# Kernel optimization log

Hardware: AMD Instinct MI355X
Metric: run time of the kernel (lower is better)

## Reference

```python
import jax, jax.numpy as jnp
import numpy as np


def setup_inputs() -> dict:
    key = jax.random.key(0)
    ks = jax.random.split(key, 7)
    B, T, K, H, A = 32, 32, 196, 512, 512
    # Xavier-normal-ish scale for square 512x512 linears
    s = float(np.sqrt(2.0 / (H + A)))
    return {
        "att_feats": jax.random.normal(ks[0], (B, K, H), jnp.float32),
        "hiddens": jax.random.normal(ks[1], (B, T, H), jnp.float32),
        "sentinel": jax.random.normal(ks[2], (B, T, H), jnp.float32),
        "Wv": jax.random.normal(ks[3], (H, A), jnp.float32) * s,
        "Wg": jax.random.normal(ks[4], (H, A), jnp.float32) * s,
        "Ws": jax.random.normal(ks[5], (H, A), jnp.float32) * s,
        "wh": jax.random.normal(ks[6], (A,), jnp.float32) * s,
    }


def reference(att_feats, hiddens, sentinel, Wv, Wg, Ws, wh):
    # Dropout treated as identity (eval mode / deterministic reference).
    cv = jnp.einsum("bkh,ha->bka", att_feats, Wv)          # [B,K,A]
    cg = jnp.einsum("bth,ha->bta", hiddens, Wg)            # [B,T,A]
    # Broadcast additive attention: [B,T,K,A]
    content_v = cv[:, None, :, :] + cg[:, :, None, :]
    z_t = jnp.einsum("btka,a->btk", jnp.tanh(content_v), wh)  # [B,T,K]
    alpha_t = jax.nn.softmax(z_t, axis=-1)                    # [B,T,K]
    c_t = jnp.einsum("btk,bkh->bth", alpha_t, att_feats)      # [B,T,H]
    # Sentinel branch
    content_s = jnp.einsum("bth,ha->bta", sentinel, Ws) + cg  # [B,T,A]
    z_ext = jnp.einsum("bta,a->bt", jnp.tanh(content_s), wh)[..., None]  # [B,T,1]
    extended = jnp.concatenate([z_t, z_ext], axis=2)          # [B,T,K+1]
    alpha_hat = jax.nn.softmax(extended, axis=-1)
    beta_t = alpha_hat[:, :, -1:]                             # [B,T,1]
    c_hat_t = beta_t * sentinel + (1.0 - beta_t) * c_t        # [B,T,H]
    return (c_hat_t, alpha_t, beta_t)
```

## Files before the change

### kernel.cpp

```cpp
#include <hip/hip_runtime.h>
#include <hip/hip_bf16.h>
#include <math.h>

#define HDIM 512
#define ADIM 512
#define BATCH 32
#define TDIM 32
#define KDIM 196
#define MROWS 8320

typedef short short8 __attribute__((ext_vector_type(8)));
typedef float floatx4 __attribute__((ext_vector_type(4)));

__device__ __forceinline__ void gl_lds16(const __hip_bfloat16* g, __hip_bfloat16* l) {
    __builtin_amdgcn_global_load_lds(
        (const __attribute__((address_space(1))) unsigned int*)(const void*)g,
        (__attribute__((address_space(3))) unsigned int*)(void*)l, 16, 0, 0);
}

__global__ __launch_bounds__(256) void convA(const float* __restrict__ att,
                                             const float* __restrict__ hid,
                                             const float* __restrict__ sen,
                                             __hip_bfloat16* __restrict__ ahi,
                                             __hip_bfloat16* __restrict__ alo) {
    const int idx = blockIdx.x * 256 + threadIdx.x;
    const int row = idx >> 7;
    float4 v;
    if (row < 6272)      v = ((const float4*)att)[idx];
    else if (row < 7296) v = ((const float4*)hid)[idx - 6272 * 128];
    else                 v = ((const float4*)sen)[idx - 7296 * 128];
    float x[4] = {v.x, v.y, v.z, v.w};
    union { __hip_bfloat16 b[4]; uint2 u; } H, L;
    #pragma unroll
    for (int i = 0; i < 4; ++i) {
        H.b[i] = __float2bfloat16(x[i]);
        L.b[i] = __float2bfloat16(x[i] - __bfloat162float(H.b[i]));
    }
    ((uint2*)ahi)[idx] = H.u;
    ((uint2*)alo)[idx] = L.u;
}

__global__ __launch_bounds__(256) void convB(const float* __restrict__ Wv,
                                             const float* __restrict__ Wg,
                                             const float* __restrict__ Ws,
                                             __hip_bfloat16* __restrict__ bthi,
                                             __hip_bfloat16* __restrict__ btlo) {
    __shared__ float tile[64][65];
    const int tid = threadIdx.x;
    const float* src = blockIdx.z == 0 ? Wv : (blockIdx.z == 1 ? Wg : Ws);
    const int k0 = blockIdx.x * 64, n0 = blockIdx.y * 64;
    #pragma unroll
    for (int i = 0; i < 16; ++i) {
        int k = (tid >> 6) * 16 + i;
        int n = tid & 63;
        tile[k][n] = src[(size_t)(k0 + k) * 512 + n0 + n];
    }
    __syncthreads();
    const size_t obase = (size_t)blockIdx.z * 262144;
    #pragma unroll
    for (int i = 0; i < 16; ++i) {
        int n = (tid >> 6) * 16 + i;
        int k = tid & 63;
        float x = tile[k][n];
        __hip_bfloat16 h = __float2bfloat16(x);
        __hip_bfloat16 l = __float2bfloat16(x - __bfloat162float(h));
        size_t o = obase + (size_t)(n0 + n) * 512 + k0 + k;
        bthi[o] = h;
        btlo[o] = l;
    }
}

__global__ __launch_bounds__(256) void gemm_bf16x3(
        const __hip_bfloat16* __restrict__ Ahi, const __hip_bfloat16* __restrict__ Alo,
        const __hip_bfloat16* __restrict__ Bthi, const __hip_bfloat16* __restrict__ Btlo,
        float* __restrict__ C) {
    __shared__ __hip_bfloat16 smem[12288];

    const int tid  = threadIdx.x;
    const int lane = tid & 63;
    const int wave = tid >> 6;
    const int wm = wave >> 1;
    const int wn = wave & 1;
    const int row0 = blockIdx.x * 64;
    const int col0 = blockIdx.y * 128;
    const int seg = (row0 < 6272) ? 0 : ((row0 < 7296) ? 1 : 2);
    const __hip_bfloat16* Bh = Bthi + (size_t)seg * 262144;
    const __hip_bfloat16* Bl = Btlo + (size_t)seg * 262144;

    floatx4 acc[2][4];
    #pragma unroll
    for (int i = 0; i < 2; ++i)
        #pragma unroll
        for (int j = 0; j < 4; ++j)
            acc[i][j] = (floatx4){0.f, 0.f, 0.f, 0.f};

    const int kq8 = (lane >> 4) << 3;

    for (int k0 = 0; k0 < 512; k0 += 32) {
        #pragma unroll
        for (int s = 0; s < 6; ++s) {
            int u = tid + (s << 8);
            __hip_bfloat16* ldst = smem + u * 8;
            const __hip_bfloat16* gsrc;
            if (u < 256)        gsrc = Ahi + (size_t)(row0 + (u >> 2)) * 512 + k0 + ((u & 3) << 3);
            else if (u < 512)   { int v = u - 256;  gsrc = Alo + (size_t)(row0 + (v >> 2)) * 512 + k0 + ((v & 3) << 3); }
            else if (u < 1024)  { int v = u - 512;  gsrc = Bh  + (size_t)(col0 + (v >> 2)) * 512 + k0 + ((v & 3) << 3); }
            else                { int v = u - 1024; gsrc = Bl  + (size_t)(col0 + (v >> 2)) * 512 + k0 + ((v & 3) << 3); }
            gl_lds16(gsrc, ldst);
        }
        asm volatile("s_waitcnt vmcnt(0)" ::: "memory");
        __syncthreads();

        short8 a_hi[2], a_lo[2], b_hi[4], b_lo[4];
        #pragma unroll
        for (int i = 0; i < 2; ++i) {
            int m = wm * 32 + i * 16 + (lane & 15);
            a_hi[i] = *(const short8*)(smem + m * 32 + kq8);
            a_lo[i] = *(const short8*)(smem + 2048 + m * 32 + kq8);
        }
        #pragma unroll
        for (int j = 0; j < 4; ++j) {
            int n = wn * 64 + j * 16 + (lane & 15);
            b_hi[j] = *(const short8*)(smem + 4096 + n * 32 + kq8);
            b_lo[j] = *(const short8*)(smem + 8192 + n * 32 + kq8);
        }

        #pragma unroll
        for (int i = 0; i < 2; ++i)
            #pragma unroll
            for (int j = 0; j < 4; ++j) {
                acc[i][j] = __builtin_amdgcn_mfma_f32_16x16x32_bf16(a_hi[i], b_hi[j], acc[i][j], 0, 0, 0);
                acc[i][j] = __builtin_amdgcn_mfma_f32_16x16x32_bf16(a_hi[i], b_lo[j], acc[i][j], 0, 0, 0);
                acc[i][j] = __builtin_amdgcn_mfma_f32_16x16x32_bf16(a_lo[i], b_hi[j], acc[i][j], 0, 0, 0);
            }
        __syncthreads();
    }

    #pragma unroll
    for (int i = 0; i < 2; ++i) {
        #pragma unroll
        for (int r = 0; r < 4; ++r) {
            int row = row0 + wm * 32 + i * 16 + ((lane >> 4) << 2) + r;
            float* cp = C + (size_t)row * 512 + col0 + wn * 64 + (lane & 15);
            #pragma unroll
            for (int j = 0; j < 4; ++j) cp[j * 16] = acc[i][j][r];
        }
    }
}

__global__ __launch_bounds__(256) void z_kernel(const float* __restrict__ cv,
                                                const float* __restrict__ cg,
                                                const float* __restrict__ cs,
                                                const float* __restrict__ wh,
                                                float* __restrict__ z_t,
                                                float* __restrict__ z_ext) {
    __shared__ float cvs[8][132];
    __shared__ float cgs[32][132];
    __shared__ float css[32][132];
    __shared__ float whs[132];
    __shared__ float2 tbl[512];

    const int kb   = blockIdx.x;
    const int b    = blockIdx.y;
    const int tid  = threadIdx.x;
    const int wave = tid >> 6;
    const int lane = tid & 63;
    const int t       = tid & 31;
    const int k_local = tid >> 5;
    const int k       = kb * 8 + k_local;
    const bool do_z = (k < KDIM);
    const bool do_s = (kb == 24) && (wave == 2) && (lane < 32);
    const bool last = (kb == 24);

    #pragma unroll
    for (int j = tid; j < 512; j += 256) {
        float x  = -8.0f + (float)j * (1.0f / 32.0f);
        float t0 = tanhf(x);
        float t1 = tanhf(x + (1.0f / 32.0f));
        tbl[j] = make_float2(t0, t1 - t0);
    }

    const int r_st = tid >> 5;
    const int q_st = tid & 31;

    float acc = 0.f, acc2 = 0.f, acc_s = 0.f, acc_s2 = 0.f;

    for (int c = 0; c < 4; ++c) {
        const int a0 = c * 128;
        __syncthreads();
        {
            int kr = kb * 8 + r_st;
            if (kr < KDIM)
                *(float4*)&cvs[r_st][4 * q_st] =
                    *(const float4*)(cv + ((size_t)b * KDIM + kr) * ADIM + a0 + 4 * q_st);
        }
        #pragma unroll
        for (int s = 0; s < 4; ++s) {
            int idx = tid + s * 256;
            int rr = idx >> 5, qq = idx & 31;
            *(float4*)&cgs[rr][4 * qq] =
                *(const float4*)(cg + ((size_t)b * TDIM + rr) * ADIM + a0 + 4 * qq);
        }
        if (last) {
            #pragma unroll
            for (int s = 0; s < 4; ++s) {
                int idx = tid + s * 256;
                int rr = idx >> 5, qq = idx & 31;
                *(float4*)&css[rr][4 * qq] =
                    *(const float4*)(cs + ((size_t)b * TDIM + rr) * ADIM + a0 + 4 * qq);
            }
        }
        if (tid < 32)
            *(float4*)&whs[4 * tid] = *(const float4*)(wh + a0 + 4 * tid);
        __syncthreads();

        if (do_z) {
            #pragma unroll 8
            for (int q = 0; q < 32; ++q) {
                float4 v  = *(const float4*)&cvs[k_local][4 * q];
                float4 g  = *(const float4*)&cgs[t][4 * q];
                float4 w4 = *(const float4*)&whs[4 * q];
                float u0 = v.x + g.x, u1 = v.y + g.y, u2 = v.z + g.z, u3 = v.w + g.w;
                float y0 = fminf(fmaxf(fmaf(u0, 32.f, 256.f), 0.f), 511.f);
                float y1 = fminf(fmaxf(fmaf(u1, 32.f, 256.f), 0.f), 511.f);
                float y2 = fminf(fmaxf(fmaf(u2, 32.f, 256.f), 0.f), 511.f);
                float y3 = fminf(fmaxf(fmaf(u3, 32.f, 256.f), 0.f), 511.f);
                int i0 = (int)y0, i1 = (int)y1, i2 = (int)y2, i3 = (int)y3;
                float f0 = y0 - (float)i0, f1 = y1 - (float)i1;
                float f2 = y2 - (float)i2, f3 = y3 - (float)i3;
                float2 s0 = tbl[i0], s1 = tbl[i1], s2 = tbl[i2], s3 = tbl[i3];
                acc  = fmaf(w4.x, fmaf(f0, s0.y, s0.x), acc);
                acc2 = fmaf(w4.y, fmaf(f1, s1.y, s1.x), acc2);
                acc  = fmaf(w4.z, fmaf(f2, s2.y, s2.x), acc);
                acc2 = fmaf(w4.w, fmaf(f3, s3.y, s3.x), acc2);
            }
        }
        if (do_s) {
            #pragma unroll 8
            for (int q = 0; q < 32; ++q) {
                float4 v  = *(const float4*)&css[lane][4 * q];
                float4 g  = *(const float4*)&cgs[lane][4 * q];
                float4 w4 = *(const float4*)&whs[4 * q];
                float u0 = v.x + g.x, u1 = v.y + g.y, u2 = v.z + g.z, u3 = v.w + g.w;
                float y0 = fminf(fmaxf(fmaf(u0, 32.f, 256.f), 0.f), 511.f);
                float y1 = fminf(fmaxf(fmaf(u1, 32.f, 256.f), 0.f), 511.f);
                float y2 = fminf(fmaxf(fmaf(u2, 32.f, 256.f), 0.f), 511.f);
                float y3 = fminf(fmaxf(fmaf(u3, 32.f, 256.f), 0.f), 511.f);
                int i0 = (int)y0, i1 = (int)y1, i2 = (int)y2, i3 = (int)y3;
                float f0 = y0 - (float)i0, f1 = y1 - (float)i1;
                float f2 = y2 - (float)i2, f3 = y3 - (float)i3;
                float2 s0 = tbl[i0], s1 = tbl[i1], s2 = tbl[i2], s3 = tbl[i3];
                acc_s  = fmaf(w4.x, fmaf(f0, s0.y, s0.x), acc_s);
                acc_s2 = fmaf(w4.y, fmaf(f1, s1.y, s1.x), acc_s2);
                acc_s  = fmaf(w4.z, fmaf(f2, s2.y, s2.x), acc_s);
                acc_s2 = fmaf(w4.w, fmaf(f3, s3.y, s3.x), acc_s2);
            }
        }
    }

    if (do_z) z_t[((size_t)b * TDIM + t) * KDIM + k] = acc + acc2;
    if (do_s) z_ext[b * TDIM + lane] = acc_s + acc_s2;
}

__global__ __launch_bounds__(256) void out_kernel(const float* __restrict__ z_t,
                                                  const float* __restrict__ z_ext,
                                                  const float* __restrict__ att,
                                                  const float* __restrict__ sen,
                                                  float* __restrict__ out_chat,
                                                  float* __restrict__ out_alpha,
                                                  float* __restrict__ out_beta) {
    __shared__ float alpha_s[4][200];
    __shared__ float beta_s[4];

    const int tg = blockIdx.x;
    const int b  = blockIdx.y;
    const int tid  = threadIdx.x;
    const int wave = tid >> 6;
    const int lane = tid & 63;
    const int t = tg * 4 + wave;

    const float* zrow = z_t + ((size_t)b * TDIM + t) * KDIM;
    float z0 = zrow[lane];
    float z1 = zrow[lane + 64];
    float z2 = zrow[lane + 128];
    float z3 = (lane < 4) ? zrow[lane + 192] : -INFINITY;

    float m = fmaxf(fmaxf(z0, z1), fmaxf(z2, z3));
    #pragma unroll
    for (int off = 32; off; off >>= 1) m = fmaxf(m, __shfl_xor(m, off, 64));

    float e0 = __expf(z0 - m), e1 = __expf(z1 - m);
    float e2 = __expf(z2 - m), e3 = (lane < 4) ? __expf(z3 - m) : 0.0f;
    float s = e0 + e1 + e2 + e3;
    #pragma unroll
    for (int off = 32; off; off >>= 1) s += __shfl_xor(s, off, 64);

    float invS = 1.0f / s;
    float a0 = e0 * invS, a1 = e1 * invS, a2 = e2 * invS, a3 = e3 * invS;

    float* arow = out_alpha + ((size_t)b * TDIM + t) * KDIM;
    alpha_s[wave][lane] = a0;        arow[lane] = a0;
    alpha_s[wave][lane + 64] = a1;   arow[lane + 64] = a1;
    alpha_s[wave][lane + 128] = a2;  arow[lane + 128] = a2;
    if (lane < 4) { alpha_s[wave][lane + 192] = a3; arow[lane + 192] = a3; }

    if (lane == 0) {
        float se = z_ext[b * TDIM + t];
        float m2 = fmaxf(m, se);
        float eext = __expf(se - m2);
        float S2 = s * __expf(m - m2) + eext;
        float beta = eext / S2;
        beta_s[wave] = beta;
        out_beta[b * TDIM + t] = beta;
    }
    __syncthreads();

    const float* attb = att + (size_t)b * KDIM * HDIM;
    float acc[4][2] = {};
    #pragma unroll 4
    for (int k = 0; k < KDIM; ++k) {
        float av0 = attb[(size_t)k * HDIM + tid];
        float av1 = attb[(size_t)k * HDIM + tid + 256];
        #pragma unroll
        for (int w = 0; w < 4; ++w) {
            float a = alpha_s[w][k];
            acc[w][0] = fmaf(a, av0, acc[w][0]);
            acc[w][1] = fmaf(a, av1, acc[w][1]);
        }
    }

    #pragma unroll
    for (int w = 0; w < 4; ++w) {
        int tt = tg * 4 + w;
        float beta = beta_s[w];
        float om = 1.0f - beta;
        size_t o = ((size_t)b * TDIM + tt) * HDIM;
        out_chat[o + tid]       = fmaf(beta, sen[o + tid],       om * acc[w][0]);
        out_chat[o + tid + 256] = fmaf(beta, sen[o + tid + 256], om * acc[w][1]);
    }
}

__global__ __launch_bounds__(256) void gemm_f32(const float* __restrict__ Amat,
                                                const float* __restrict__ Bmat,
                                                float* __restrict__ Cmat) {
    __shared__ float As[16][64 + 4];
    __shared__ float Bs[16][64];
    const int tid = threadIdx.x;
    const int tx = tid & 15;
    const int ty = tid >> 4;
    const int row0 = blockIdx.x * 64;
    const int col0 = blockIdx.y * 64;
    float acc[4][4] = {};
    for (int k0 = 0; k0 < HDIM; k0 += 16) {
        #pragma unroll
        for (int i = 0; i < 4; ++i) {
            int idx = tid + i * 256;
            As[idx & 15][idx >> 4] = Amat[(size_t)(row0 + (idx >> 4)) * HDIM + k0 + (idx & 15)];
        }
        #pragma unroll
        for (int i = 0; i < 4; ++i) {
            int idx = tid + i * 256;
            Bs[idx >> 6][idx & 63] = Bmat[(size_t)(k0 + (idx >> 6)) * ADIM + col0 + (idx & 63)];
        }
        __syncthreads();
        #pragma unroll
        for (int k = 0; k < 16; ++k) {
            float4 a4 = *(const float4*)&As[k][ty * 4];
            float4 b4 = *(const float4*)&Bs[k][tx * 4];
            float a[4] = {a4.x, a4.y, a4.z, a4.w};
            float b[4] = {b4.x, b4.y, b4.z, b4.w};
            #pragma unroll
            for (int i = 0; i < 4; ++i)
                #pragma unroll
                for (int j = 0; j < 4; ++j)
                    acc[i][j] += a[i] * b[j];
        }
        __syncthreads();
    }
    #pragma unroll
    for (int i = 0; i < 4; ++i) {
        size_t r = (size_t)(row0 + ty * 4 + i) * ADIM + col0 + tx * 4;
        #pragma unroll
        for (int j = 0; j < 4; ++j) Cmat[r + j] = acc[i][j];
    }
}

extern "C" void kernel_launch(void* const* d_in, const int* in_sizes, int n_in,
                              void* d_out, int out_size, void* d_ws, size_t ws_size,
                              hipStream_t stream) {
    const float* att = (const float*)d_in[0];
    const float* hid = (const float*)d_in[1];
    const float* sen = (const float*)d_in[2];
    const float* Wv  = (const float*)d_in[3];
    const float* Wg  = (const float*)d_in[4];
    const float* Ws  = (const float*)d_in[5];
    const float* wh  = (const float*)d_in[6];

    float* out = (float*)d_out;
    float* out_chat  = out;
    float* out_alpha = out + 524288;
    float* out_beta  = out + 524288 + 200704;

    char* wsb = (char*)d_ws;
    const size_t C_BYTES  = (size_t)MROWS * 512 * 4;
    const size_t ZT_BYTES = 200704 * 4;
    const size_t ZE_BYTES = 4096;
    const size_t AH_BYTES = (size_t)MROWS * 512 * 2;
    const size_t BT_BYTES = (size_t)3 * 512 * 512 * 2;
    const size_t need = C_BYTES + ZT_BYTES + ZE_BYTES + 2 * AH_BYTES + 2 * BT_BYTES;

    float* C  = (float*)wsb;
    float* cv = C;
    float* cg = C + 6272 * 512;
    float* cs = C + 7296 * 512;
    float* zt = (float*)(wsb + C_BYTES);
    float* ze = (float*)(wsb + C_BYTES + ZT_BYTES);

    if (ws_size >= need) {
        __hip_bfloat16* ahi  = (__hip_bfloat16*)(wsb + C_BYTES + ZT_BYTES + ZE_BYTES);
        __hip_bfloat16* alo  = ahi + (size_t)MROWS * 512;
        __hip_bfloat16* bthi = alo + (size_t)MROWS * 512;
        __hip_bfloat16* btlo = bthi + (size_t)3 * 512 * 512;

        convA<<<4160, 256, 0, stream>>>(att, hid, sen, ahi, alo);
        convB<<<dim3(8, 8, 3), 256, 0, stream>>>(Wv, Wg, Ws, bthi, btlo);
        gemm_bf16x3<<<dim3(130, 4), 256, 0, stream>>>(ahi, alo, bthi, btlo, C);
    } else {
        gemm_f32<<<dim3(98, 8), 256, 0, stream>>>(att, Wv, cv);
        gemm_f32<<<dim3(16, 8), 256, 0, stream>>>(hid, Wg, cg);
        gemm_f32<<<dim3(16, 8), 256, 0, stream>>>(sen, Ws, cs);
    }

    z_kernel<<<dim3(25, 32), 256, 0, stream>>>(cv, cg, cs, wh, zt, ze);

    out_kernel<<<dim3(8, 32), 256, 0, stream>>>(zt, ze, att, sen,
                                                out_chat, out_alpha, out_beta);
}
```

Baseline: 177.2 us.

## Fuse conversion kernels, use exp2-based tanh, move sentinel score into output kernel

Merges the activation and weight bf16 split-conversion kernels into one launch. Replaces the LDS tanh lookup table with an exp2/rcp tanh, with the 2*log2(e) factor folded into the GEMM epilogue. Moves the sentinel score computation out of the last z_kernel block into out_kernel via a wave reduction. This removes a launch, the table setup and the serialized sentinel tail, at the cost of more transcendental instructions per element.

```diff
diff --git a/kernel.cpp b/kernel.cpp
--- a/kernel.cpp
+++ b/kernel.cpp
@@ -8,6 +8,7 @@
 #define TDIM 32
 #define KDIM 196
 #define MROWS 8320
+#define ZSC 2.885390081777927f
 
 typedef short short8 __attribute__((ext_vector_type(8)));
 typedef float floatx4 __attribute__((ext_vector_type(4)));
@@ -18,55 +19,67 @@
         (__attribute__((address_space(3))) unsigned int*)(void*)l, 16, 0, 0);
 }
 
-__global__ __launch_bounds__(256) void convA(const float* __restrict__ att,
-                                             const float* __restrict__ hid,
-                                             const float* __restrict__ sen,
-                                             __hip_bfloat16* __restrict__ ahi,
-                                             __hip_bfloat16* __restrict__ alo) {
-    const int idx = blockIdx.x * 256 + threadIdx.x;
-    const int row = idx >> 7;
-    float4 v;
-    if (row < 6272)      v = ((const float4*)att)[idx];
-    else if (row < 7296) v = ((const float4*)hid)[idx - 6272 * 128];
-    else                 v = ((const float4*)sen)[idx - 7296 * 128];
-    float x[4] = {v.x, v.y, v.z, v.w};
-    union { __hip_bfloat16 b[4]; uint2 u; } H, L;
-    #pragma unroll
-    for (int i = 0; i < 4; ++i) {
-        H.b[i] = __float2bfloat16(x[i]);
-        L.b[i] = __float2bfloat16(x[i] - __bfloat162float(H.b[i]));
-    }
-    ((uint2*)ahi)[idx] = H.u;
-    ((uint2*)alo)[idx] = L.u;
-}
-
-__global__ __launch_bounds__(256) void convB(const float* __restrict__ Wv,
-                                             const float* __restrict__ Wg,
-                                             const float* __restrict__ Ws,
-                                             __hip_bfloat16* __restrict__ bthi,
-                                             __hip_bfloat16* __restrict__ btlo) {
+__device__ __forceinline__ float tanh_ps(float up) {
+    float e = __builtin_amdgcn_exp2f(up);
+    float r = __builtin_amdgcn_rcpf(e + 1.0f);
+    return fmaf(-2.0f, r, 1.0f);
+}
+
+__global__ __launch_bounds__(256) void conv_fused(const float* __restrict__ att,
+                                                  const float* __restrict__ hid,
+                                                  const float* __restrict__ sen,
+                                                  const float* __restrict__ Wv,
+                                                  const float* __restrict__ Wg,
+                                                  const float* __restrict__ Ws,
+                                                  __hip_bfloat16* __restrict__ ahi,
+                                                  __hip_bfloat16* __restrict__ alo,
+                                                  __hip_bfloat16* __restrict__ bthi,
+                                                  __hip_bfloat16* __restrict__ btlo) {
     __shared__ float tile[64][65];
     const int tid = threadIdx.x;
-    const float* src = blockIdx.z == 0 ? Wv : (blockIdx.z == 1 ? Wg : Ws);
-    const int k0 = blockIdx.x * 64, n0 = blockIdx.y * 64;
-    #pragma unroll
-    for (int i = 0; i < 16; ++i) {
-        int k = (tid >> 6) * 16 + i;
-        int n = tid & 63;
-        tile[k][n] = src[(size_t)(k0 + k) * 512 + n0 + n];
-    }
-    __syncthreads();
-    const size_t obase = (size_t)blockIdx.z * 262144;
-    #pragma unroll
-    for (int i = 0; i < 16; ++i) {
-        int n = (tid >> 6) * 16 + i;
-        int k = tid & 63;
-        float x = tile[k][n];
-        __hip_bfloat16 h = __float2bfloat16(x);
-        __hip_bfloat16 l = __float2bfloat16(x - __bfloat162float(h));
-        size_t o = obase + (size_t)(n0 + n) * 512 + k0 + k;
-        bthi[o] = h;
-        btlo[o] = l;
+
+    if (blockIdx.x < 4160) {
+        const int idx = blockIdx.x * 256 + tid;
+        const int row = idx >> 7;
+        float4 v;
+        if (row < 6272)      v = ((const float4*)att)[idx];
+        else if (row < 7296) v = ((const float4*)hid)[idx - 6272 * 128];
+        else                 v = ((const float4*)sen)[idx - 7296 * 128];
+        float x[4] = {v.x, v.y, v.z, v.w};
+        union { __hip_bfloat16 b[4]; uint2 u; } H, L;
+        #pragma unroll
+        for (int i = 0; i < 4; ++i) {
+            H.b[i] = __float2bfloat16(x[i]);
+            L.b[i] = __float2bfloat16(x[i] - __bfloat162float(H.b[i]));
+        }
+        ((uint2*)ahi)[idx] = H.u;
+        ((uint2*)alo)[idx] = L.u;
+    } else {
+        const int bid = blockIdx.x - 4160;
+        const int mz  = bid >> 6;
+        const int rem = bid & 63;
+        const int k0  = (rem >> 3) * 64;
+        const int n0  = (rem & 7) * 64;
+        const float* src = mz == 0 ? Wv : (mz == 1 ? Wg : Ws);
+        #pragma unroll
+        for (int i = 0; i < 16; ++i) {
+            int k = (tid >> 6) * 16 + i;
+            int n = tid & 63;
+            tile[k][n] = src[(size_t)(k0 + k) * 512 + n0 + n];
+        }
+        __syncthreads();
+        const size_t obase = (size_t)mz * 262144;
+        #pragma unroll
+        for (int i = 0; i < 16; ++i) {
+            int n = (tid >> 6) * 16 + i;
+            int k = tid & 63;
+            float x = tile[k][n];
+            __hip_bfloat16 h = __float2bfloat16(x);
+            __hip_bfloat16 l = __float2bfloat16(x - __bfloat162float(h));
+            size_t o = obase + (size_t)(n0 + n) * 512 + k0 + k;
+            bthi[o] = h;
+            btlo[o] = l;
+        }
     }
 }
 
@@ -143,47 +156,31 @@
             int row = row0 + wm * 32 + i * 16 + ((lane >> 4) << 2) + r;
             float* cp = C + (size_t)row * 512 + col0 + wn * 64 + (lane & 15);
             #pragma unroll
-            for (int j = 0; j < 4; ++j) cp[j * 16] = acc[i][j][r];
+            for (int j = 0; j < 4; ++j) cp[j * 16] = acc[i][j][r] * ZSC;
         }
     }
 }
 
 __global__ __launch_bounds__(256) void z_kernel(const float* __restrict__ cv,
                                                 const float* __restrict__ cg,
-                                                const float* __restrict__ cs,
                                                 const float* __restrict__ wh,
-                                                float* __restrict__ z_t,
-                                                float* __restrict__ z_ext) {
+                                                float* __restrict__ z_t) {
     __shared__ float cvs[8][132];
     __shared__ float cgs[32][132];
-    __shared__ float css[32][132];
     __shared__ float whs[132];
-    __shared__ float2 tbl[512];
-
-    const int kb   = blockIdx.x;
-    const int b    = blockIdx.y;
-    const int tid  = threadIdx.x;
-    const int wave = tid >> 6;
-    const int lane = tid & 63;
+
+    const int kb  = blockIdx.x;
+    const int b   = blockIdx.y;
+    const int tid = threadIdx.x;
     const int t       = tid & 31;
     const int k_local = tid >> 5;
     const int k       = kb * 8 + k_local;
     const bool do_z = (k < KDIM);
-    const bool do_s = (kb == 24) && (wave == 2) && (lane < 32);
-    const bool last = (kb == 24);
-
-    #pragma unroll
-    for (int j = tid; j < 512; j += 256) {
-        float x  = -8.0f + (float)j * (1.0f / 32.0f);
-        float t0 = tanhf(x);
-        float t1 = tanhf(x + (1.0f / 32.0f));
-        tbl[j] = make_float2(t0, t1 - t0);
-    }
 
     const int r_st = tid >> 5;
     const int q_st = tid & 31;
 
-    float acc = 0.f, acc2 = 0.f, acc_s = 0.f, acc_s2 = 0.f;
+    float acc = 0.f, acc2 = 0.f;
 
     for (int c = 0; c < 4; ++c) {
         const int a0 = c * 128;
@@ -200,15 +197,6 @@
             int rr = idx >> 5, qq = idx & 31;
             *(float4*)&cgs[rr][4 * qq] =
                 *(const float4*)(cg + ((size_t)b * TDIM + rr) * ADIM + a0 + 4 * qq);
-        }
-        if (last) {
-            #pragma unroll
-            for (int s = 0; s < 4; ++s) {
-                int idx = tid + s * 256;
-                int rr = idx >> 5, qq = idx & 31;
-                *(float4*)&css[rr][4 * qq] =
-                    *(const float4*)(cs + ((size_t)b * TDIM + rr) * ADIM + a0 + 4 * qq);
-            }
         }
         if (tid < 32)
             *(float4*)&whs[4 * tid] = *(const float4*)(wh + a0 + 4 * tid);
@@ -220,50 +208,21 @@
                 float4 v  = *(const float4*)&cvs[k_local][4 * q];
                 float4 g  = *(const float4*)&cgs[t][4 * q];
                 float4 w4 = *(const float4*)&whs[4 * q];
-                float u0 = v.x + g.x, u1 = v.y + g.y, u2 = v.z + g.z, u3 = v.w + g.w;
-                float y0 = fminf(fmaxf(fmaf(u0, 32.f, 256.f), 0.f), 511.f);
-                float y1 = fminf(fmaxf(fmaf(u1, 32.f, 256.f), 0.f), 511.f);
-                float y2 = fminf(fmaxf(fmaf(u2, 32.f, 256.f), 0.f), 511.f);
-                float y3 = fminf(fmaxf(fmaf(u3, 32.f, 256.f), 0.f), 511.f);
-                int i0 = (int)y0, i1 = (int)y1, i2 = (int)y2, i3 = (int)y3;
-                float f0 = y0 - (float)i0, f1 = y1 - (float)i1;
-                float f2 = y2 - (float)i2, f3 = y3 - (float)i3;
-                float2 s0 = tbl[i0], s1 = tbl[i1], s2 = tbl[i2], s3 = tbl[i3];
-                acc  = fmaf(w4.x, fmaf(f0, s0.y, s0.x), acc);
-                acc2 = fmaf(w4.y, fmaf(f1, s1.y, s1.x), acc2);
-                acc  = fmaf(w4.z, fmaf(f2, s2.y, s2.x), acc);
-                acc2 = fmaf(w4.w, fmaf(f3, s3.y, s3.x), acc2);
+                acc  = fmaf(w4.x, tanh_ps(v.x + g.x), acc);
+                acc2 = fmaf(w4.y, tanh_ps(v.y + g.y), acc2);
+                acc  = fmaf(w4.z, tanh_ps(v.z + g.z), acc);
+                acc2 = fmaf(w4.w, tanh_ps(v.w + g.w), acc2);
             }
         }
-        if (do_s) {
-            #pragma unroll 8
-            for (int q = 0; q < 32; ++q) {
-                float4 v  = *(const float4*)&css[lane][4 * q];
-                float4 g  = *(const float4*)&cgs[lane][4 * q];
-                float4 w4 = *(const float4*)&whs[4 * q];
-                float u0 = v.x + g.x, u1 = v.y + g.y, u2 = v.z + g.z, u3 = v.w + g.w;
-                float y0 = fminf(fmaxf(fmaf(u0, 32.f, 256.f), 0.f), 511.f);
-                float y1 = fminf(fmaxf(fmaf(u1, 32.f, 256.f), 0.f), 511.f);
-                float y2 = fminf(fmaxf(fmaf(u2, 32.f, 256.f), 0.f), 511.f);
-                float y3 = fminf(fmaxf(fmaf(u3, 32.f, 256.f), 0.f), 511.f);
-                int i0 = (int)y0, i1 = (int)y1, i2 = (int)y2, i3 = (int)y3;
-                float f0 = y0 - (float)i0, f1 = y1 - (float)i1;
-                float f2 = y2 - (float)i2, f3 = y3 - (float)i3;
-                float2 s0 = tbl[i0], s1 = tbl[i1], s2 = tbl[i2], s3 = tbl[i3];
-                acc_s  = fmaf(w4.x, fmaf(f0, s0.y, s0.x), acc_s);
-                acc_s2 = fmaf(w4.y, fmaf(f1, s1.y, s1.x), acc_s2);
-                acc_s  = fmaf(w4.z, fmaf(f2, s2.y, s2.x), acc_s);
-                acc_s2 = fmaf(w4.w, fmaf(f3, s3.y, s3.x), acc_s2);
-            }
-        }
     }
 
     if (do_z) z_t[((size_t)b * TDIM + t) * KDIM + k] = acc + acc2;
-    if (do_s) z_ext[b * TDIM + lane] = acc_s + acc_s2;
 }
 
 __global__ __launch_bounds__(256) void out_kernel(const float* __restrict__ z_t,
-                                                  const float* __restrict__ z_ext,
+                                                  const float* __restrict__ cs,
+                                                  const float* __restrict__ cg,
+                                                  const float* __restrict__ wh,
                                                   const float* __restrict__ att,
                                                   const float* __restrict__ sen,
                                                   float* __restrict__ out_chat,
@@ -279,6 +238,23 @@
     const int lane = tid & 63;
     const int t = tg * 4 + wave;
 
+    const float* csrow = cs + ((size_t)b * TDIM + t) * ADIM;
+    const float* cgrow = cg + ((size_t)b * TDIM + t) * ADIM;
+    float p = 0.f;
+    #pragma unroll
+    for (int h = 0; h < 2; ++h) {
+        float4 sv = *(const float4*)(csrow + 8 * lane + 4 * h);
+        float4 gv = *(const float4*)(cgrow + 8 * lane + 4 * h);
+        float4 w4 = *(const float4*)(wh + 8 * lane + 4 * h);
+        p = fmaf(w4.x, tanh_ps(sv.x + gv.x), p);
+        p = fmaf(w4.y, tanh_ps(sv.y + gv.y), p);
+        p = fmaf(w4.z, tanh_ps(sv.z + gv.z), p);
+        p = fmaf(w4.w, tanh_ps(sv.w + gv.w), p);
+    }
+    #pragma unroll
+    for (int off = 32; off; off >>= 1) p += __shfl_xor(p, off, 64);
+    const float se = p;
+
     const float* zrow = z_t + ((size_t)b * TDIM + t) * KDIM;
     float z0 = zrow[lane];
     float z1 = zrow[lane + 64];
@@ -304,12 +280,11 @@
     alpha_s[wave][lane + 128] = a2;  arow[lane + 128] = a2;
     if (lane < 4) { alpha_s[wave][lane + 192] = a3; arow[lane + 192] = a3; }
 
+    float m2 = fmaxf(m, se);
+    float eext = __expf(se - m2);
+    float S2 = s * __expf(m - m2) + eext;
+    float beta = eext / S2;
     if (lane == 0) {
-        float se = z_ext[b * TDIM + t];
-        float m2 = fmaxf(m, se);
-        float eext = __expf(se - m2);
-        float S2 = s * __expf(m - m2) + eext;
-        float beta = eext / S2;
         beta_s[wave] = beta;
         out_beta[b * TDIM + t] = beta;
     }
@@ -332,11 +307,11 @@
     #pragma unroll
     for (int w = 0; w < 4; ++w) {
         int tt = tg * 4 + w;
-        float beta = beta_s[w];
-        float om = 1.0f - beta;
+        float bt = beta_s[w];
+        float om = 1.0f - bt;
         size_t o = ((size_t)b * TDIM + tt) * HDIM;
-        out_chat[o + tid]       = fmaf(beta, sen[o + tid],       om * acc[w][0]);
-        out_chat[o + tid + 256] = fmaf(beta, sen[o + tid + 256], om * acc[w][1]);
+        out_chat[o + tid]       = fmaf(bt, sen[o + tid],       om * acc[w][0]);
+        out_chat[o + tid + 256] = fmaf(bt, sen[o + tid + 256], om * acc[w][1]);
     }
 }
 
@@ -381,7 +356,7 @@
     for (int i = 0; i < 4; ++i) {
         size_t r = (size_t)(row0 + ty * 4 + i) * ADIM + col0 + tx * 4;
         #pragma unroll
-        for (int j = 0; j < 4; ++j) Cmat[r + j] = acc[i][j];
+        for (int j = 0; j < 4; ++j) Cmat[r + j] = acc[i][j] * ZSC;
     }
 }
 
@@ -404,26 +379,24 @@
     char* wsb = (char*)d_ws;
     const size_t C_BYTES  = (size_t)MROWS * 512 * 4;
     const size_t ZT_BYTES = 200704 * 4;
-    const size_t ZE_BYTES = 4096;
     const size_t AH_BYTES = (size_t)MROWS * 512 * 2;
     const size_t BT_BYTES = (size_t)3 * 512 * 512 * 2;
-    const size_t need = C_BYTES + ZT_BYTES + ZE_BYTES + 2 * AH_BYTES + 2 * BT_BYTES;
+    const size_t need = C_BYTES + ZT_BYTES + 2 * AH_BYTES + 2 * BT_BYTES;
 
     float* C  = (float*)wsb;
     float* cv = C;
     float* cg = C + 6272 * 512;
     float* cs = C + 7296 * 512;
     float* zt = (float*)(wsb + C_BYTES);
-    float* ze = (float*)(wsb + C_BYTES + ZT_BYTES);
 
     if (ws_size >= need) {
-        __hip_bfloat16* ahi  = (__hip_bfloat16*)(wsb + C_BYTES + ZT_BYTES + ZE_BYTES);
+        __hip_bfloat16* ahi  = (__hip_bfloat16*)(wsb + C_BYTES + ZT_BYTES);
         __hip_bfloat16* alo  = ahi + (size_t)MROWS * 512;
         __hip_bfloat16* bthi = alo + (size_t)MROWS * 512;
         __hip_bfloat16* btlo = bthi + (size_t)3 * 512 * 512;
 
-        convA<<<4160, 256, 0, stream>>>(att, hid, sen, ahi, alo);
-        convB<<<dim3(8, 8, 3), 256, 0, stream>>>(Wv, Wg, Ws, bthi, btlo);
+        conv_fused<<<4352, 256, 0, stream>>>(att, hid, sen, Wv, Wg, Ws,
+                                             ahi, alo, bthi, btlo);
         gemm_bf16x3<<<dim3(130, 4), 256, 0, stream>>>(ahi, alo, bthi, btlo, C);
     } else {
         gemm_f32<<<dim3(98, 8), 256, 0, stream>>>(att, Wv, cv);
@@ -431,8 +404,8 @@
         gemm_f32<<<dim3(16, 8), 256, 0, stream>>>(sen, Ws, cs);
     }
 
-    z_kernel<<<dim3(25, 32), 256, 0, stream>>>(cv, cg, cs, wh, zt, ze);
-
-    out_kernel<<<dim3(8, 32), 256, 0, stream>>>(zt, ze, att, sen,
+    z_kernel<<<dim3(25, 32), 256, 0, stream>>>(cv, cg, wh, zt);
+
+    out_kernel<<<dim3(8, 32), 256, 0, stream>>>(zt, cs, cg, wh, att, sen,
                                                 out_chat, out_alpha, out_beta);
 }
```

After: 161.4 us. 1.1x faster.
